# Optimization experiments

Hardware: AMD Instinct MI355X
Metric: run time of the kernel (lower is better)

The kernel has to match this reference:

```python
import jax, jax.numpy as jnp
import numpy as np
from jax import lax

H = 1028  # hidden_size


def _lstm_layer(x, w_ih, w_hh, b_ih, b_hh):
    # x: [B, T, in], w_ih: [4H, in], w_hh: [4H, H] (PyTorch gate order i,f,g,o)
    B, T, _ = x.shape
    h_dim = w_hh.shape[1]
    # Precompute input contribution for all timesteps (memory-bound GEMM)
    xg = jnp.einsum('bti,gi->btg', x, w_ih) + b_ih + b_hh  # [B, T, 4H]

    def step(carry, xt):
        h, c = carry
        g = xt + h @ w_hh.T  # [B, 4H]
        i, f, gg, o = jnp.split(g, 4, axis=-1)
        i = jax.nn.sigmoid(i)
        f = jax.nn.sigmoid(f)
        gg = jnp.tanh(gg)
        o = jax.nn.sigmoid(o)
        c = f * c + i * gg
        h = o * jnp.tanh(c)
        return (h, c), h

    h0 = jnp.zeros((B, h_dim), x.dtype)
    c0 = jnp.zeros((B, h_dim), x.dtype)
    _, hs = lax.scan(step, (h0, c0), jnp.swapaxes(xg, 0, 1))  # [T, B, H]
    return jnp.swapaxes(hs, 0, 1)  # [B, T, H]


def setup_inputs() -> dict:
    key = jax.random.key(0)
    ks = jax.random.split(key, 12)
    s = 1.0 / np.sqrt(H)  # torch LSTM/Linear init scale

    def u(k, shape):
        return jax.random.uniform(k, shape, jnp.float32, -s, s)

    x = jax.random.normal(ks[0], (1, 16384, 1), dtype=jnp.float32)
    return {
        'x': x,
        'w_ih0': u(ks[1], (4 * H, 1)),
        'w_hh0': u(ks[2], (4 * H, H)),
        'b_ih0': u(ks[3], (4 * H,)),
        'b_hh0': u(ks[4], (4 * H,)),
        'w_ih1': u(ks[5], (4 * H, H)),
        'w_hh1': u(ks[6], (4 * H, H)),
        'b_ih1': u(ks[7], (4 * H,)),
        'b_hh1': u(ks[8], (4 * H,)),
        'lin_w': u(ks[9], (1, H)),
        'lin_b': u(ks[10], (1,)),
    }


def reference(x, w_ih0, w_hh0, b_ih0, b_hh0, w_ih1, w_hh1, b_ih1, b_hh1, lin_w, lin_b):
    h1 = _lstm_layer(x, w_ih0, w_hh0, b_ih0, b_hh0)   # [B, T, H]
    h2 = _lstm_layer(h1, w_ih1, w_hh1, b_ih1, b_hh1)  # [B, T, H]
    return h2 @ lin_w.T + lin_b                        # [B, T, 1]
```

## Files before the change

kernel.cpp:

```cpp
#include <hip/hip_runtime.h>
#include <math.h>

#define HH    1028
#define TT    16384
#define UP    1056
#define HSU   1056
#define HS    1056
#define NWG0  66
#define NWG1  132
#define NWGT  (NWG0 + NWG1)
#define R0    1024
#define R0M   (R0 - 1)
#define R1M   15

typedef unsigned long long u64;

__device__ __forceinline__ u64 ld_u64(const u64* p) {
    return __hip_atomic_load(p, __ATOMIC_RELAXED, __HIP_MEMORY_SCOPE_AGENT);
}
__device__ __forceinline__ void st_u64(u64* p, u64 v) {
    __hip_atomic_store(p, v, __ATOMIC_RELAXED, __HIP_MEMORY_SCOPE_AGENT);
}
__device__ __forceinline__ unsigned ld_u32(const unsigned* p) {
    return __hip_atomic_load(p, __ATOMIC_RELAXED, __HIP_MEMORY_SCOPE_AGENT);
}
__device__ __forceinline__ void st_u32(unsigned* p, unsigned v) {
    __hip_atomic_store(p, v, __ATOMIC_RELAXED, __HIP_MEMORY_SCOPE_AGENT);
}
__device__ __forceinline__ float sigmf(float x) { return 1.0f / (1.0f + expf(-x)); }
__device__ __forceinline__ u64 pack(unsigned tag, float v) {
    return ((u64)tag << 32) | (u64)__float_as_uint(v);
}

__device__ __forceinline__ void stage132(const u64* __restrict__ src, float* __restrict__ lds,
                                         int base, int lane, unsigned want, long long& budget) {
    const int i0 = base + lane, i1 = base + 64 + lane, i2 = base + 128 + lane;
    bool d0 = false, d1 = false, d2 = (lane >= 4);
    for (;;) {
        if (!d0) { u64 v = ld_u64(src + i0);
                   if ((unsigned)(v >> 32) == want) { lds[i0] = __uint_as_float((unsigned)v); d0 = true; } }
        if (!d1) { u64 v = ld_u64(src + i1);
                   if ((unsigned)(v >> 32) == want) { lds[i1] = __uint_as_float((unsigned)v); d1 = true; } }
        if (!d2) { u64 v = ld_u64(src + i2);
                   if ((unsigned)(v >> 32) == want) { lds[i2] = __uint_as_float((unsigned)v); d2 = true; } }
        if (__all(d0 & d1 & d2)) break;
        if (--budget < 0) break;
        __builtin_amdgcn_s_sleep(1);
    }
}

__device__ __forceinline__ void stage264(const u64* __restrict__ src, float* __restrict__ lds,
                                         int base, int lane, unsigned want, long long& budget) {
    const int i0 = base + lane, i1 = i0 + 64, i2 = i0 + 128, i3 = i0 + 192, i4 = i0 + 256;
    bool d0 = false, d1 = false, d2 = false, d3 = false, d4 = (lane >= 8);
    for (;;) {
        if (!d0) { u64 v = ld_u64(src + i0);
                   if ((unsigned)(v >> 32) == want) { lds[i0] = __uint_as_float((unsigned)v); d0 = true; } }
        if (!d1) { u64 v = ld_u64(src + i1);
                   if ((unsigned)(v >> 32) == want) { lds[i1] = __uint_as_float((unsigned)v); d1 = true; } }
        if (!d2) { u64 v = ld_u64(src + i2);
                   if ((unsigned)(v >> 32) == want) { lds[i2] = __uint_as_float((unsigned)v); d2 = true; } }
        if (!d3) { u64 v = ld_u64(src + i3);
                   if ((unsigned)(v >> 32) == want) { lds[i3] = __uint_as_float((unsigned)v); d3 = true; } }
        if (!d4) { u64 v = ld_u64(src + i4);
                   if ((unsigned)(v >> 32) == want) { lds[i4] = __uint_as_float((unsigned)v); d4 = true; } }
        if (__all(d0 & d1 & d2 & d3 & d4)) break;
        if (--budget < 0) break;
        __builtin_amdgcn_s_sleep(1);
    }
}

__global__ __launch_bounds__(1024, 4) void wn_fused(
    const float* __restrict__ x,
    const float* __restrict__ w_ih0, const float* __restrict__ w_hh0,
    const float* __restrict__ b_ih0, const float* __restrict__ b_hh0,
    const float* __restrict__ w_ih1, const float* __restrict__ w_hh1,
    const float* __restrict__ b_ih1, const float* __restrict__ b_hh1,
    u64* __restrict__ ring0,
    u64* __restrict__ ring1,
    float* __restrict__ h2hist,
    unsigned* __restrict__ l1prog)
{
    __shared__ float smem[4 * UP + 128];
    const int tid  = threadIdx.x;
    const int lane = tid & 63;
    const int w    = tid >> 6;

    for (int i = tid; i < 4 * UP + 128; i += 1024) smem[i] = 0.0f;

    if (blockIdx.x < NWG0) {
        float* hbuf = smem;
        float* gbuf = smem + 2 * UP;
        const int wg   = blockIdx.x;
        const int row  = tid >> 4;
        const int k0   = tid & 15;
        const int gate = row >> 4;
        const int du   = row & 15;
        const int u    = wg * 16 + du;
        const bool real = (u < HH);
        const int wr   = gate * HH + (real ? u : 0);

        float wv[16][4], wt0 = 0.f, wt1 = 0.f;
#pragma unroll
        for (int m = 0; m < 16; ++m) {
            const int j = k0 * 4 + m * 64;
#pragma unroll
            for (int q = 0; q < 4; ++q)
                wv[m][q] = (real && j + q < HH) ? w_hh0[(size_t)wr * HH + j + q] : 0.0f;
        }
        {   const int j = 1024 + k0 * 2;
            wt0 = (real && j     < HH) ? w_hh0[(size_t)wr * HH + j]     : 0.0f;
            wt1 = (real && j + 1 < HH) ? w_hh0[(size_t)wr * HH + j + 1] : 0.0f; }
#pragma unroll
        for (int m = 0; m < 16; ++m)
#pragma unroll
            for (int q = 0; q < 4; ++q) asm volatile("" : "+v"(wv[m][q]));
        asm volatile("" : "+v"(wt0), "+v"(wt1));

        const float wx = real ? w_ih0[wr] : 0.0f;
        const float bs = real ? (b_ih0[wr] + b_hh0[wr]) : 0.0f;
        __syncthreads();

        long long budget = 20000000LL;
        float c_reg = 0.0f;
        for (int t = 0; t < TT; ++t) {
            if (t > 0) {
                if (w == 0) {
                    const float* gl = gbuf + ((t - 1) & 1) * 64;
                    if (lane < 16) {
                        const float gi = gl[lane], gf = gl[16 + lane];
                        const float gg = gl[32 + lane], go = gl[48 + lane];
                        const float iv = sigmf(gi), fv = sigmf(gf), gv = tanhf(gg), ov = sigmf(go);
                        c_reg = fv * c_reg + iv * gv;
                        float hv = ov * tanhf(c_reg);
                        if (wg * 16 + lane >= HH) hv = 0.0f;
                        st_u64(ring0 + (size_t)((t - 1) & R0M) * HSU + wg * 16 + lane,
                               pack((unsigned)t, hv));
                    }
                } else if (w >= 4 && w < 12) {
                    stage132(ring0 + (size_t)((t - 1) & R0M) * HSU, hbuf + (t & 1) * UP,
                             (w - 4) * 132, lane, (unsigned)t, budget);
                } else if (w == 1 && lane == 0 && (t & 255) == 0) {
                    for (;;) {
                        unsigned p = ld_u32(l1prog);
                        if ((int)t - (int)p < R0 - 256) break;
                        if (--budget < 0) break;
                        __builtin_amdgcn_s_sleep(32);
                    }
                }
            }
            __syncthreads();
            const float* hb = hbuf + (t & 1) * UP;
            float acc = 0.0f;
#pragma unroll
            for (int m = 0; m < 16; ++m) {
                const float4 hv = *(const float4*)&hb[k0 * 4 + m * 64];
                acc = fmaf(wv[m][0], hv.x, acc);
                acc = fmaf(wv[m][1], hv.y, acc);
                acc = fmaf(wv[m][2], hv.z, acc);
                acc = fmaf(wv[m][3], hv.w, acc);
            }
            {   const float2 hv = *(const float2*)&hb[1024 + k0 * 2];
                acc = fmaf(wt0, hv.x, acc);
                acc = fmaf(wt1, hv.y, acc); }
#pragma unroll
            for (int off = 1; off < 16; off <<= 1) acc += __shfl_xor(acc, off);
            if (k0 == 0) gbuf[(t & 1) * 64 + row] = acc + x[t] * wx + bs;
            __syncthreads();
        }
        if (w == 0 && lane < 16) {
            const float* gl = gbuf + ((TT - 1) & 1) * 64;
            const float gi = gl[lane], gf = gl[16 + lane];
            const float gg = gl[32 + lane], go = gl[48 + lane];
            const float iv = sigmf(gi), fv = sigmf(gf), gv = tanhf(gg), ov = sigmf(go);
            c_reg = fv * c_reg + iv * gv;
            float hv = ov * tanhf(c_reg);
            if (wg * 16 + lane >= HH) hv = 0.0f;
            st_u64(ring0 + (size_t)((TT - 1) & R0M) * HSU + wg * 16 + lane,
                   pack((unsigned)TT, hv));
        }
    } else {
        float* abuf = smem;
        float* bbuf = smem + 2 * UP;
        float* gbuf = smem + 4 * UP;
        const int wg   = blockIdx.x - NWG0;
        const int row  = tid >> 5;
        const int k0   = tid & 31;
        const int gate = row >> 3;
        const int du   = row & 7;
        const int u    = wg * 8 + du;
        const bool real = (u < HH);
        const int wr   = gate * HH + (real ? u : 0);

        float wiv[8][4], whv[8][4], wit = 0.f, wht = 0.f;
#pragma unroll
        for (int m = 0; m < 8; ++m) {
            const int j = k0 * 4 + m * 128;
#pragma unroll
            for (int q = 0; q < 4; ++q) {
                const bool inb = real && (j + q < HH);
                wiv[m][q] = inb ? w_ih1[(size_t)wr * HH + j + q] : 0.0f;
                whv[m][q] = inb ? w_hh1[(size_t)wr * HH + j + q] : 0.0f;
            }
        }
        {   const int j = 1024 + k0;
            wit = (real && j < HH) ? w_ih1[(size_t)wr * HH + j] : 0.0f;
            wht = (real && j < HH) ? w_hh1[(size_t)wr * HH + j] : 0.0f; }
#pragma unroll
        for (int m = 0; m < 8; ++m)
#pragma unroll
            for (int q = 0; q < 4; ++q) {
                asm volatile("" : "+v"(wiv[m][q]));
                asm volatile("" : "+v"(whv[m][q]));
            }
        asm volatile("" : "+v"(wit), "+v"(wht));
        const float bs = real ? (b_ih1[wr] + b_hh1[wr]) : 0.0f;
        __syncthreads();

        long long budget = 20000000LL;
        float c_reg = 0.0f;
        for (int t = 0; t < TT; ++t) {
            if (w == 0) {
                if (t > 0) {
                    const float* gl = gbuf + ((t - 1) & 1) * 32;
                    if (lane < 8) {
                        const float gi = gl[lane], gf = gl[8 + lane];
                        const float gg = gl[16 + lane], go = gl[24 + lane];
                        const float iv = sigmf(gi), fv = sigmf(gf), gv = tanhf(gg), ov = sigmf(go);
                        c_reg = fv * c_reg + iv * gv;
                        float hv = ov * tanhf(c_reg);
                        if (wg * 8 + lane >= HH) hv = 0.0f;
                        st_u64(ring1 + (size_t)((t - 1) & R1M) * HSU + wg * 8 + lane,
                               pack((unsigned)t, hv));
                        h2hist[(size_t)(t - 1) * HS + wg * 8 + lane] = hv;
                    }
                }
            } else if (w >= 4 && w < 12) {
                if (t > 0)
                    stage132(ring1 + (size_t)((t - 1) & R1M) * HSU, bbuf + (t & 1) * UP,
                             (w - 4) * 132, lane, (unsigned)t, budget);
            } else if (w >= 12) {
                stage264(ring0 + (size_t)(t & R0M) * HSU, abuf + (t & 1) * UP,
                         (w - 12) * 264, lane, (unsigned)(t + 1), budget);
            }
            __syncthreads();
            const float* ab = abuf + (t & 1) * UP;
            const float* bb = bbuf + (t & 1) * UP;
            float acc = 0.0f;
#pragma unroll
            for (int m = 0; m < 8; ++m) {
                const float4 ha = *(const float4*)&ab[k0 * 4 + m * 128];
                const float4 hb2 = *(const float4*)&bb[k0 * 4 + m * 128];
                acc = fmaf(wiv[m][0], ha.x, acc);
                acc = fmaf(wiv[m][1], ha.y, acc);
                acc = fmaf(wiv[m][2], ha.z, acc);
                acc = fmaf(wiv[m][3], ha.w, acc);
                acc = fmaf(whv[m][0], hb2.x, acc);
                acc = fmaf(whv[m][1], hb2.y, acc);
                acc = fmaf(whv[m][2], hb2.z, acc);
                acc = fmaf(whv[m][3], hb2.w, acc);
            }
            acc = fmaf(wit, ab[1024 + k0], acc);
            acc = fmaf(wht, bb[1024 + k0], acc);
#pragma unroll
            for (int off = 1; off < 32; off <<= 1) acc += __shfl_xor(acc, off);
            if (k0 == 0) gbuf[(t & 1) * 32 + row] = acc + bs;
            __syncthreads();
            if (w == 1 && lane == 0 && wg == 0 && (t & 255) == 255)
                st_u32(l1prog, (unsigned)(t + 1));
        }
        if (w == 0 && lane < 8) {
            const float* gl = gbuf + ((TT - 1) & 1) * 32;
            const float gi = gl[lane], gf = gl[8 + lane];
            const float gg = gl[16 + lane], go = gl[24 + lane];
            const float iv = sigmf(gi), fv = sigmf(gf), gv = tanhf(gg), ov = sigmf(go);
            c_reg = fv * c_reg + iv * gv;
            float hv = ov * tanhf(c_reg);
            if (wg * 8 + lane >= HH) hv = 0.0f;
            h2hist[(size_t)(TT - 1) * HS + wg * 8 + lane] = hv;
        }
    }
}

__global__ __launch_bounds__(256) void wn_proj(
    const float* __restrict__ h2,
    const float* __restrict__ lin_w,
    const float* __restrict__ lin_b,
    float* __restrict__ out)
{
    const int lane = threadIdx.x & 63;
    const int wv   = threadIdx.x >> 6;
    const int t    = blockIdx.x * 4 + wv;
    const float* hp = h2 + (size_t)t * HS;
    float acc = 0.0f;
#pragma unroll
    for (int m = 0; m < 4; ++m) {
        const int j = lane * 4 + m * 256;
        const float4 h4 = *(const float4*)(hp + j);
        const float4 w4 = *(const float4*)(lin_w + j);
        acc += h4.x * w4.x + h4.y * w4.y + h4.z * w4.z + h4.w * w4.w;
    }
    if (lane == 0) {
#pragma unroll
        for (int j = 1024; j < HH; ++j) acc += hp[j] * lin_w[j];
    }
#pragma unroll
    for (int off = 1; off < 64; off <<= 1) acc += __shfl_xor(acc, off);
    if (lane == 0) out[t] = acc + lin_b[0];
}

extern "C" void kernel_launch(void* const* d_in, const int* in_sizes, int n_in,
                              void* d_out, int out_size, void* d_ws, size_t ws_size,
                              hipStream_t stream) {
    const float* x     = (const float*)d_in[0];
    const float* w_ih0 = (const float*)d_in[1];
    const float* w_hh0 = (const float*)d_in[2];
    const float* b_ih0 = (const float*)d_in[3];
    const float* b_hh0 = (const float*)d_in[4];
    const float* w_ih1 = (const float*)d_in[5];
    const float* w_hh1 = (const float*)d_in[6];
    const float* b_ih1 = (const float*)d_in[7];
    const float* b_hh1 = (const float*)d_in[8];
    const float* lin_w = (const float*)d_in[9];
    const float* lin_b = (const float*)d_in[10];
    float* out = (float*)d_out;

    char* ws = (char*)d_ws;
    const size_t R0B = (size_t)R0 * HSU * 8;
    const size_t R1B = (size_t)16 * HSU * 8;
    const size_t H2B = (size_t)TT * HS * 4;
    u64* ring0 = (u64*)(ws);
    u64* ring1 = (u64*)(ws + R0B);
    float* h2hist = (float*)(ws + R0B + R1B);
    unsigned* l1prog = (unsigned*)(ws + R0B + R1B + H2B);

    wn_fused<<<NWGT, 1024, 0, stream>>>(x, w_ih0, w_hh0, b_ih0, b_hh0,
                                        w_ih1, w_hh1, b_ih1, b_hh1,
                                        ring0, ring1, h2hist, l1prog);
    wn_proj<<<TT / 4, 256, 0, stream>>>(h2hist, lin_w, lin_b, out);
}
```

Baseline: 43.45 ms.

## Halve workgroup size, compute LSTM cell per wave, publish h via LDS tag slots

Workgroups shrink from 1024 to 512 threads. Each wave now computes complete gate rows for its own hidden units (two units per wave in layer 0, one in layer 1) and evaluates the cell nonlinearity in-register with shuffles. This removes the gate buffer and the second __syncthreads per timestep, replacing it with tagged LDS slots that wave 0 polls before forwarding h to the global ring. All waves now share the staging of the ring into LDS. Each thread holds twice as many weight registers, and LDS spin-polling adds latency on the serial critical path.

After: 54.83 ms. +26.2%, slower.

```diff
diff --git a/kernel.cpp b/kernel.cpp
--- a/kernel.cpp
+++ b/kernel.cpp
@@ -26,6 +26,12 @@
 }
 __device__ __forceinline__ void st_u32(unsigned* p, unsigned v) {
     __hip_atomic_store(p, v, __ATOMIC_RELAXED, __HIP_MEMORY_SCOPE_AGENT);
+}
+__device__ __forceinline__ u64 lds_ld(const u64* p) {
+    return __hip_atomic_load(p, __ATOMIC_RELAXED, __HIP_MEMORY_SCOPE_WORKGROUP);
+}
+__device__ __forceinline__ void lds_st(u64* p, u64 v) {
+    __hip_atomic_store(p, v, __ATOMIC_RELAXED, __HIP_MEMORY_SCOPE_WORKGROUP);
 }
 __device__ __forceinline__ float sigmf(float x) { return 1.0f / (1.0f + expf(-x)); }
 __device__ __forceinline__ u64 pack(unsigned tag, float v) {
@@ -70,7 +76,20 @@
     }
 }
 
-__global__ __launch_bounds__(1024, 4) void wn_fused(
+__device__ __forceinline__ u64 gatherN(const u64* slots, int lane, int n, unsigned want,
+                                       long long& budget) {
+    u64 v = 0; bool done = (lane >= n);
+    for (;;) {
+        if (!done) { v = lds_ld(slots + lane);
+                     done = ((unsigned)(v >> 32) == want); }
+        if (__all(done)) break;
+        if (--budget < 0) break;
+        __builtin_amdgcn_s_sleep(1);
+    }
+    return v;
+}
+
+__global__ __launch_bounds__(512, 2) void wn_fused(
     const float* __restrict__ x,
     const float* __restrict__ w_ih0, const float* __restrict__ w_hh0,
     const float* __restrict__ b_ih0, const float* __restrict__ b_hh0,
@@ -81,66 +100,64 @@
     float* __restrict__ h2hist,
     unsigned* __restrict__ l1prog)
 {
-    __shared__ float smem[4 * UP + 128];
+    __shared__ float smem[4 * UP];
+    __shared__ u64 hslot[16];
     const int tid  = threadIdx.x;
     const int lane = tid & 63;
     const int w    = tid >> 6;
-
-    for (int i = tid; i < 4 * UP + 128; i += 1024) smem[i] = 0.0f;
+    const int gate = (lane >> 4) & 3;
+    const int k0   = lane & 15;
+
+    for (int i = tid; i < 4 * UP; i += 512) smem[i] = 0.0f;
+    if (tid < 16) hslot[tid] = 0;
 
     if (blockIdx.x < NWG0) {
         float* hbuf = smem;
-        float* gbuf = smem + 2 * UP;
-        const int wg   = blockIdx.x;
-        const int row  = tid >> 4;
-        const int k0   = tid & 15;
-        const int gate = row >> 4;
-        const int du   = row & 15;
-        const int u    = wg * 16 + du;
-        const bool real = (u < HH);
-        const int wr   = gate * HH + (real ? u : 0);
-
-        float wv[16][4], wt0 = 0.f, wt1 = 0.f;
+        const int wg = blockIdx.x;
+        const int u0 = wg * 16 + 2 * w;
+        const int u1 = u0 + 1;
+        const bool r0 = (u0 < HH), r1 = (u1 < HH);
+        const int wr0 = gate * HH + (r0 ? u0 : 0);
+        const int wr1 = gate * HH + (r1 ? u1 : 0);
+
+        float wa[16][4], wb[16][4], wta0 = 0.f, wta1 = 0.f, wtb0 = 0.f, wtb1 = 0.f;
 #pragma unroll
         for (int m = 0; m < 16; ++m) {
             const int j = k0 * 4 + m * 64;
 #pragma unroll
-            for (int q = 0; q < 4; ++q)
-                wv[m][q] = (real && j + q < HH) ? w_hh0[(size_t)wr * HH + j + q] : 0.0f;
+            for (int q = 0; q < 4; ++q) {
+                wa[m][q] = (r0 && j + q < HH) ? w_hh0[(size_t)wr0 * HH + j + q] : 0.0f;
+                wb[m][q] = (r1 && j + q < HH) ? w_hh0[(size_t)wr1 * HH + j + q] : 0.0f;
+            }
         }
         {   const int j = 1024 + k0 * 2;
-            wt0 = (real && j     < HH) ? w_hh0[(size_t)wr * HH + j]     : 0.0f;
-            wt1 = (real && j + 1 < HH) ? w_hh0[(size_t)wr * HH + j + 1] : 0.0f; }
+            wta0 = (r0 && j     < HH) ? w_hh0[(size_t)wr0 * HH + j]     : 0.0f;
+            wta1 = (r0 && j + 1 < HH) ? w_hh0[(size_t)wr0 * HH + j + 1] : 0.0f;
+            wtb0 = (r1 && j     < HH) ? w_hh0[(size_t)wr1 * HH + j]     : 0.0f;
+            wtb1 = (r1 && j + 1 < HH) ? w_hh0[(size_t)wr1 * HH + j + 1] : 0.0f; }
 #pragma unroll
         for (int m = 0; m < 16; ++m)
 #pragma unroll
-            for (int q = 0; q < 4; ++q) asm volatile("" : "+v"(wv[m][q]));
-        asm volatile("" : "+v"(wt0), "+v"(wt1));
-
-        const float wx = real ? w_ih0[wr] : 0.0f;
-        const float bs = real ? (b_ih0[wr] + b_hh0[wr]) : 0.0f;
+            for (int q = 0; q < 4; ++q) {
+                asm volatile("" : "+v"(wa[m][q]));
+                asm volatile("" : "+v"(wb[m][q]));
+            }
+        asm volatile("" : "+v"(wta0), "+v"(wta1), "+v"(wtb0), "+v"(wtb1));
+
+        const float wx0 = r0 ? w_ih0[wr0] : 0.0f;
+        const float bs0 = r0 ? (b_ih0[wr0] + b_hh0[wr0]) : 0.0f;
+        const float wx1 = r1 ? w_ih0[wr1] : 0.0f;
+        const float bs1 = r1 ? (b_ih0[wr1] + b_hh0[wr1]) : 0.0f;
         __syncthreads();
 
         long long budget = 20000000LL;
-        float c_reg = 0.0f;
+        float c0 = 0.0f, c1 = 0.0f;
         for (int t = 0; t < TT; ++t) {
             if (t > 0) {
                 if (w == 0) {
-                    const float* gl = gbuf + ((t - 1) & 1) * 64;
-                    if (lane < 16) {
-                        const float gi = gl[lane], gf = gl[16 + lane];
-                        const float gg = gl[32 + lane], go = gl[48 + lane];
-                        const float iv = sigmf(gi), fv = sigmf(gf), gv = tanhf(gg), ov = sigmf(go);
-                        c_reg = fv * c_reg + iv * gv;
-                        float hv = ov * tanhf(c_reg);
-                        if (wg * 16 + lane >= HH) hv = 0.0f;
-                        st_u64(ring0 + (size_t)((t - 1) & R0M) * HSU + wg * 16 + lane,
-                               pack((unsigned)t, hv));
-                    }
-                } else if (w >= 4 && w < 12) {
-                    stage132(ring0 + (size_t)((t - 1) & R0M) * HSU, hbuf + (t & 1) * UP,
-                             (w - 4) * 132, lane, (unsigned)t, budget);
-                } else if (w == 1 && lane == 0 && (t & 255) == 0) {
+                    u64 v = gatherN(hslot, lane, 16, (unsigned)t, budget);
+                    if (lane < 16) st_u64(ring0 + (size_t)((t - 1) & R0M) * HSU + wg * 16 + lane, v);
+                } else if (w == 1 && lane == 63 && (t & 255) == 0) {
                     for (;;) {
                         unsigned p = ld_u32(l1prog);
                         if ((int)t - (int)p < R0 - 256) break;
@@ -148,54 +165,72 @@
                         __builtin_amdgcn_s_sleep(32);
                     }
                 }
+                stage132(ring0 + (size_t)((t - 1) & R0M) * HSU, hbuf + (t & 1) * UP,
+                         w * 132, lane, (unsigned)t, budget);
             }
             __syncthreads();
             const float* hb = hbuf + (t & 1) * UP;
-            float acc = 0.0f;
+            float a0 = 0.0f, a1 = 0.0f;
 #pragma unroll
             for (int m = 0; m < 16; ++m) {
                 const float4 hv = *(const float4*)&hb[k0 * 4 + m * 64];
-                acc = fmaf(wv[m][0], hv.x, acc);
-                acc = fmaf(wv[m][1], hv.y, acc);
-                acc = fmaf(wv[m][2], hv.z, acc);
-                acc = fmaf(wv[m][3], hv.w, acc);
+                a0 = fmaf(wa[m][0], hv.x, a0);
+                a0 = fmaf(wa[m][1], hv.y, a0);
+                a0 = fmaf(wa[m][2], hv.z, a0);
+                a0 = fmaf(wa[m][3], hv.w, a0);
+                a1 = fmaf(wb[m][0], hv.x, a1);
+                a1 = fmaf(wb[m][1], hv.y, a1);
+                a1 = fmaf(wb[m][2], hv.z, a1);
+                a1 = fmaf(wb[m][3], hv.w, a1);
             }
             {   const float2 hv = *(const float2*)&hb[1024 + k0 * 2];
-                acc = fmaf(wt0, hv.x, acc);
-                acc = fmaf(wt1, hv.y, acc); }
-#pragma unroll
-            for (int off = 1; off < 16; off <<= 1) acc += __shfl_xor(acc, off);
-            if (k0 == 0) gbuf[(t & 1) * 64 + row] = acc + x[t] * wx + bs;
-            __syncthreads();
-        }
-        if (w == 0 && lane < 16) {
-            const float* gl = gbuf + ((TT - 1) & 1) * 64;
-            const float gi = gl[lane], gf = gl[16 + lane];
-            const float gg = gl[32 + lane], go = gl[48 + lane];
-            const float iv = sigmf(gi), fv = sigmf(gf), gv = tanhf(gg), ov = sigmf(go);
-            c_reg = fv * c_reg + iv * gv;
-            float hv = ov * tanhf(c_reg);
-            if (wg * 16 + lane >= HH) hv = 0.0f;
-            st_u64(ring0 + (size_t)((TT - 1) & R0M) * HSU + wg * 16 + lane,
-                   pack((unsigned)TT, hv));
+                a0 = fmaf(wta0, hv.x, a0);
+                a0 = fmaf(wta1, hv.y, a0);
+                a1 = fmaf(wtb0, hv.x, a1);
+                a1 = fmaf(wtb1, hv.y, a1); }
+#pragma unroll
+            for (int off = 1; off < 16; off <<= 1) {
+                a0 += __shfl_xor(a0, off);
+                a1 += __shfl_xor(a1, off);
+            }
+            const float xt = x[t];
+            if (k0 == 0) {
+                a0 += xt * wx0 + bs0;
+                a1 += xt * wx1 + bs1;
+            }
+            {   const float gi = __shfl(a0, 0),  gf = __shfl(a0, 16);
+                const float gg = __shfl(a0, 32), go = __shfl(a0, 48);
+                const float iv = sigmf(gi), fv = sigmf(gf), gv = tanhf(gg), ov = sigmf(go);
+                c0 = fv * c0 + iv * gv;
+                float hv0 = ov * tanhf(c0);
+                if (!r0) hv0 = 0.0f;
+                if (lane == 0) lds_st(&hslot[2 * w], pack((unsigned)(t + 1), hv0));
+            }
+            {   const float gi = __shfl(a1, 0),  gf = __shfl(a1, 16);
+                const float gg = __shfl(a1, 32), go = __shfl(a1, 48);
+                const float iv = sigmf(gi), fv = sigmf(gf), gv = tanhf(gg), ov = sigmf(go);
+                c1 = fv * c1 + iv * gv;
+                float hv1 = ov * tanhf(c1);
+                if (!r1) hv1 = 0.0f;
+                if (lane == 0) lds_st(&hslot[2 * w + 1], pack((unsigned)(t + 1), hv1));
+            }
+        }
+        if (w == 0) {
+            u64 v = gatherN(hslot, lane, 16, (unsigned)TT, budget);
+            if (lane < 16) st_u64(ring0 + (size_t)((TT - 1) & R0M) * HSU + wg * 16 + lane, v);
         }
     } else {
         float* abuf = smem;
         float* bbuf = smem + 2 * UP;
-        float* gbuf = smem + 4 * UP;
-        const int wg   = blockIdx.x - NWG0;
-        const int row  = tid >> 5;
-        const int k0   = tid & 31;
-        const int gate = row >> 3;
-        const int du   = row & 7;
-        const int u    = wg * 8 + du;
+        const int wg = blockIdx.x - NWG0;
+        const int u  = wg * 8 + w;
         const bool real = (u < HH);
-        const int wr   = gate * HH + (real ? u : 0);
-
-        float wiv[8][4], whv[8][4], wit = 0.f, wht = 0.f;
-#pragma unroll
-        for (int m = 0; m < 8; ++m) {
-            const int j = k0 * 4 + m * 128;
+        const int wr = gate * HH + (real ? u : 0);
+
+        float wiv[16][4], whv[16][4], wi0 = 0.f, wi1 = 0.f, wh0 = 0.f, wh1 = 0.f;
+#pragma unroll
+        for (int m = 0; m < 16; ++m) {
+            const int j = k0 * 4 + m * 64;
 #pragma unroll
             for (int q = 0; q < 4; ++q) {
                 const bool inb = real && (j + q < HH);
@@ -203,81 +238,82 @@
                 whv[m][q] = inb ? w_hh1[(size_t)wr * HH + j + q] : 0.0f;
             }
         }
-        {   const int j = 1024 + k0;
-            wit = (real && j < HH) ? w_ih1[(size_t)wr * HH + j] : 0.0f;
-            wht = (real && j < HH) ? w_hh1[(size_t)wr * HH + j] : 0.0f; }
-#pragma unroll
-        for (int m = 0; m < 8; ++m)
+        {   const int j = 1024 + k0 * 2;
+            wi0 = (real && j     < HH) ? w_ih1[(size_t)wr * HH + j]     : 0.0f;
+            wi1 = (real && j + 1 < HH) ? w_ih1[(size_t)wr * HH + j + 1] : 0.0f;
+            wh0 = (real && j     < HH) ? w_hh1[(size_t)wr * HH + j]     : 0.0f;
+            wh1 = (real && j + 1 < HH) ? w_hh1[(size_t)wr * HH + j + 1] : 0.0f; }
+#pragma unroll
+        for (int m = 0; m < 16; ++m)
 #pragma unroll
             for (int q = 0; q < 4; ++q) {
                 asm volatile("" : "+v"(wiv[m][q]));
                 asm volatile("" : "+v"(whv[m][q]));
             }
-        asm volatile("" : "+v"(wit), "+v"(wht));
+        asm volatile("" : "+v"(wi0), "+v"(wi1), "+v"(wh0), "+v"(wh1));
         const float bs = real ? (b_ih1[wr] + b_hh1[wr]) : 0.0f;
         __syncthreads();
 
         long long budget = 20000000LL;
         float c_reg = 0.0f;
         for (int t = 0; t < TT; ++t) {
-            if (w == 0) {
-                if (t > 0) {
-                    const float* gl = gbuf + ((t - 1) & 1) * 32;
-                    if (lane < 8) {
-                        const float gi = gl[lane], gf = gl[8 + lane];
-                        const float gg = gl[16 + lane], go = gl[24 + lane];
-                        const float iv = sigmf(gi), fv = sigmf(gf), gv = tanhf(gg), ov = sigmf(go);
-                        c_reg = fv * c_reg + iv * gv;
-                        float hv = ov * tanhf(c_reg);
-                        if (wg * 8 + lane >= HH) hv = 0.0f;
-                        st_u64(ring1 + (size_t)((t - 1) & R1M) * HSU + wg * 8 + lane,
-                               pack((unsigned)t, hv));
-                        h2hist[(size_t)(t - 1) * HS + wg * 8 + lane] = hv;
-                    }
+            if (w == 0 && t > 0) {
+                u64 v = gatherN(hslot, lane, 8, (unsigned)t, budget);
+                if (lane < 8) {
+                    st_u64(ring1 + (size_t)((t - 1) & R1M) * HSU + wg * 8 + lane, v);
+                    h2hist[(size_t)(t - 1) * HS + wg * 8 + lane] = __uint_as_float((unsigned)v);
                 }
-            } else if (w >= 4 && w < 12) {
+            }
+            if (w < 4) {
                 if (t > 0)
-                    stage132(ring1 + (size_t)((t - 1) & R1M) * HSU, bbuf + (t & 1) * UP,
-                             (w - 4) * 132, lane, (unsigned)t, budget);
-            } else if (w >= 12) {
+                    stage264(ring1 + (size_t)((t - 1) & R1M) * HSU, bbuf + (t & 1) * UP,
+                             w * 264, lane, (unsigned)t, budget);
+            } else {
                 stage264(ring0 + (size_t)(t & R0M) * HSU, abuf + (t & 1) * UP,
-                         (w - 12) * 264, lane, (unsigned)(t + 1), budget);
+                         (w - 4) * 264, lane, (unsigned)(t + 1), budget);
             }
             __syncthreads();
             const float* ab = abuf + (t & 1) * UP;
             const float* bb = bbuf + (t & 1) * UP;
             float acc = 0.0f;
 #pragma unroll
-            for (int m = 0; m < 8; ++m) {
-                const float4 ha = *(const float4*)&ab[k0 * 4 + m * 128];
-                const float4 hb2 = *(const float4*)&bb[k0 * 4 + m * 128];
+            for (int m = 0; m < 16; ++m) {
+                const float4 ha = *(const float4*)&ab[k0 * 4 + m * 64];
+                const float4 hb = *(const float4*)&bb[k0 * 4 + m * 64];
                 acc = fmaf(wiv[m][0], ha.x, acc);
                 acc = fmaf(wiv[m][1], ha.y, acc);
                 acc = fmaf(wiv[m][2], ha.z, acc);
                 acc = fmaf(wiv[m][3], ha.w, acc);
-                acc = fmaf(whv[m][0], hb2.x, acc);
-                acc = fmaf(whv[m][1], hb2.y, acc);
-                acc = fmaf(whv[m][2], hb2.z, acc);
-                acc = fmaf(whv[m][3], hb2.w, acc);
-            }
-            acc = fmaf(wit, ab[1024 + k0], acc);
-            acc = fmaf(wht, bb[1024 + k0], acc);
-#pragma unroll
-            for (int off = 1; off < 32; off <<= 1) acc += __shfl_xor(acc, off);
-            if (k0 == 0) gbuf[(t & 1) * 32 + row] = acc + bs;
-            __syncthreads();
-            if (w == 1 && lane == 0 && wg == 0 && (t & 255) == 255)
-                st_u32(l1prog, (unsigned)(t + 1));
-        }
-        if (w == 0 && lane < 8) {
-            const float* gl = gbuf + ((TT - 1) & 1) * 32;
-            const float gi = gl[lane], gf = gl[8 + lane];
-            const float gg = gl[16 + lane], go = gl[24 + lane];
+                acc = fmaf(whv[m][0], hb.x, acc);
+                acc = fmaf(whv[m][1], hb.y, acc);
+                acc = fmaf(whv[m][2], hb.z, acc);
+                acc = fmaf(whv[m][3], hb.w, acc);
+            }
+            {   const float2 ha = *(const float2*)&ab[1024 + k0 * 2];
+                const float2 hb = *(const float2*)&bb[1024 + k0 * 2];
+                acc = fmaf(wi0, ha.x, acc);
+                acc = fmaf(wi1, ha.y, acc);
+                acc = fmaf(wh0, hb.x, acc);
+                acc = fmaf(wh1, hb.y, acc); }
+#pragma unroll
+            for (int off = 1; off < 16; off <<= 1) acc += __shfl_xor(acc, off);
+            if (k0 == 0) acc += bs;
+            const float gi = __shfl(acc, 0);
+            const float gf = __shfl(acc, 16);
+            const float gg = __shfl(acc, 32);
+            const float go = __shfl(acc, 48);
             const float iv = sigmf(gi), fv = sigmf(gf), gv = tanhf(gg), ov = sigmf(go);
             c_reg = fv * c_reg + iv * gv;
             float hv = ov * tanhf(c_reg);
-            if (wg * 8 + lane >= HH) hv = 0.0f;
-            h2hist[(size_t)(TT - 1) * HS + wg * 8 + lane] = hv;
+            if (!real) hv = 0.0f;
+            if (lane == 0) lds_st(&hslot[w], pack((unsigned)(t + 1), hv));
+            if (w == 7 && lane == 63 && wg == 0 && (t & 255) == 255)
+                st_u32(l1prog, (unsigned)(t + 1));
+        }
+        if (w == 0) {
+            u64 v = gatherN(hslot, lane, 8, (unsigned)TT, budget);
+            if (lane < 8)
+                h2hist[(size_t)(TT - 1) * HS + wg * 8 + lane] = __uint_as_float((unsigned)v);
         }
     }
 }
@@ -334,8 +370,8 @@
     float* h2hist = (float*)(ws + R0B + R1B);
     unsigned* l1prog = (unsigned*)(ws + R0B + R1B + H2B);
 
-    wn_fused<<<NWGT, 1024, 0, stream>>>(x, w_ih0, w_hh0, b_ih0, b_hh0,
-                                        w_ih1, w_hh1, b_ih1, b_hh1,
-                                        ring0, ring1, h2hist, l1prog);
+    wn_fused<<<NWGT, 512, 0, stream>>>(x, w_ih0, w_hh0, b_ih0, b_hh0,
+                                       w_ih1, w_hh1, b_ih1, b_hh1,
+                                       ring0, ring1, h2hist, l1prog);
     wn_proj<<<TT / 4, 256, 0, stream>>>(h2hist, lin_w, lin_b, out);
 }
```

## Replace second per-step barrier with tagged LDS gate slots and widen staging

Applied to the files above, without the earlier changes.

Drops the second __syncthreads per timestep in both LSTM layers. Gate sums are now written as tag+value 64-bit words into LDS slots, and wave 0 spin-polls those slots and gathers the gates with shuffles. Staging of the global h ring is spread over 11 waves with 96 elements each instead of 8 waves with 132, and the l1prog progress store moves to a staging wave. The aim is to cut the barrier latency on the serial recurrence critical path. The cost is LDS polling and a greater reliance on relaxed workgroup-scope ordering to stay correct.

Result: no change. 43.66 ms (+0.5%).

```diff
diff --git a/kernel.cpp b/kernel.cpp
--- a/kernel.cpp
+++ b/kernel.cpp
@@ -27,23 +27,27 @@
 __device__ __forceinline__ void st_u32(unsigned* p, unsigned v) {
     __hip_atomic_store(p, v, __ATOMIC_RELAXED, __HIP_MEMORY_SCOPE_AGENT);
 }
+__device__ __forceinline__ u64 lds_ld(const u64* p) {
+    return __hip_atomic_load(p, __ATOMIC_RELAXED, __HIP_MEMORY_SCOPE_WORKGROUP);
+}
+__device__ __forceinline__ void lds_st(u64* p, u64 v) {
+    __hip_atomic_store(p, v, __ATOMIC_RELAXED, __HIP_MEMORY_SCOPE_WORKGROUP);
+}
 __device__ __forceinline__ float sigmf(float x) { return 1.0f / (1.0f + expf(-x)); }
 __device__ __forceinline__ u64 pack(unsigned tag, float v) {
     return ((u64)tag << 32) | (u64)__float_as_uint(v);
 }
 
-__device__ __forceinline__ void stage132(const u64* __restrict__ src, float* __restrict__ lds,
-                                         int base, int lane, unsigned want, long long& budget) {
-    const int i0 = base + lane, i1 = base + 64 + lane, i2 = base + 128 + lane;
-    bool d0 = false, d1 = false, d2 = (lane >= 4);
+__device__ __forceinline__ void stage96(const u64* __restrict__ src, float* __restrict__ lds,
+                                        int base, int lane, unsigned want, long long& budget) {
+    const int i0 = base + lane, i1 = base + 64 + lane;
+    bool d0 = false, d1 = (lane >= 32);
     for (;;) {
         if (!d0) { u64 v = ld_u64(src + i0);
                    if ((unsigned)(v >> 32) == want) { lds[i0] = __uint_as_float((unsigned)v); d0 = true; } }
         if (!d1) { u64 v = ld_u64(src + i1);
                    if ((unsigned)(v >> 32) == want) { lds[i1] = __uint_as_float((unsigned)v); d1 = true; } }
-        if (!d2) { u64 v = ld_u64(src + i2);
-                   if ((unsigned)(v >> 32) == want) { lds[i2] = __uint_as_float((unsigned)v); d2 = true; } }
-        if (__all(d0 & d1 & d2)) break;
+        if (__all(d0 & d1)) break;
         if (--budget < 0) break;
         __builtin_amdgcn_s_sleep(1);
     }
@@ -70,6 +74,19 @@
     }
 }
 
+__device__ __forceinline__ float pollslots(const u64* slots, int lane, int n, unsigned want,
+                                           long long& budget) {
+    u64 v = 0; bool done = (lane >= n);
+    for (;;) {
+        if (!done) { v = lds_ld(slots + lane);
+                     done = ((unsigned)(v >> 32) == want); }
+        if (__all(done)) break;
+        if (--budget < 0) break;
+        __builtin_amdgcn_s_sleep(1);
+    }
+    return __uint_as_float((unsigned)v);
+}
+
 __global__ __launch_bounds__(1024, 4) void wn_fused(
     const float* __restrict__ x,
     const float* __restrict__ w_ih0, const float* __restrict__ w_hh0,
@@ -81,16 +98,17 @@
     float* __restrict__ h2hist,
     unsigned* __restrict__ l1prog)
 {
-    __shared__ float smem[4 * UP + 128];
+    __shared__ float smem[4 * UP];
+    __shared__ u64 gslot[2 * 64];
     const int tid  = threadIdx.x;
     const int lane = tid & 63;
     const int w    = tid >> 6;
 
-    for (int i = tid; i < 4 * UP + 128; i += 1024) smem[i] = 0.0f;
+    for (int i = tid; i < 4 * UP; i += 1024) smem[i] = 0.0f;
+    if (tid < 128) gslot[tid] = 0;
 
     if (blockIdx.x < NWG0) {
         float* hbuf = smem;
-        float* gbuf = smem + 2 * UP;
         const int wg   = blockIdx.x;
         const int row  = tid >> 4;
         const int k0   = tid & 15;
@@ -126,10 +144,12 @@
         for (int t = 0; t < TT; ++t) {
             if (t > 0) {
                 if (w == 0) {
-                    const float* gl = gbuf + ((t - 1) & 1) * 64;
+                    float gsum = pollslots(gslot + ((t - 1) & 1) * 64, lane, 64, (unsigned)t, budget);
+                    const float gi = __shfl(gsum, lane & 15);
+                    const float gf = __shfl(gsum, 16 + (lane & 15));
+                    const float gg = __shfl(gsum, 32 + (lane & 15));
+                    const float go = __shfl(gsum, 48 + (lane & 15));
                     if (lane < 16) {
-                        const float gi = gl[lane], gf = gl[16 + lane];
-                        const float gg = gl[32 + lane], go = gl[48 + lane];
                         const float iv = sigmf(gi), fv = sigmf(gf), gv = tanhf(gg), ov = sigmf(go);
                         c_reg = fv * c_reg + iv * gv;
                         float hv = ov * tanhf(c_reg);
@@ -137,10 +157,10 @@
                         st_u64(ring0 + (size_t)((t - 1) & R0M) * HSU + wg * 16 + lane,
                                pack((unsigned)t, hv));
                     }
-                } else if (w >= 4 && w < 12) {
-                    stage132(ring0 + (size_t)((t - 1) & R0M) * HSU, hbuf + (t & 1) * UP,
-                             (w - 4) * 132, lane, (unsigned)t, budget);
-                } else if (w == 1 && lane == 0 && (t & 255) == 0) {
+                } else if (w >= 1 && w < 12) {
+                    stage96(ring0 + (size_t)((t - 1) & R0M) * HSU, hbuf + (t & 1) * UP,
+                            (w - 1) * 96, lane, (unsigned)t, budget);
+                } else if (w == 12 && lane == 0 && (t & 255) == 0) {
                     for (;;) {
                         unsigned p = ld_u32(l1prog);
                         if ((int)t - (int)p < R0 - 256) break;
@@ -165,24 +185,28 @@
                 acc = fmaf(wt1, hv.y, acc); }
 #pragma unroll
             for (int off = 1; off < 16; off <<= 1) acc += __shfl_xor(acc, off);
-            if (k0 == 0) gbuf[(t & 1) * 64 + row] = acc + x[t] * wx + bs;
-            __syncthreads();
-        }
-        if (w == 0 && lane < 16) {
-            const float* gl = gbuf + ((TT - 1) & 1) * 64;
-            const float gi = gl[lane], gf = gl[16 + lane];
-            const float gg = gl[32 + lane], go = gl[48 + lane];
-            const float iv = sigmf(gi), fv = sigmf(gf), gv = tanhf(gg), ov = sigmf(go);
-            c_reg = fv * c_reg + iv * gv;
-            float hv = ov * tanhf(c_reg);
-            if (wg * 16 + lane >= HH) hv = 0.0f;
-            st_u64(ring0 + (size_t)((TT - 1) & R0M) * HSU + wg * 16 + lane,
-                   pack((unsigned)TT, hv));
+            if (k0 == 0)
+                lds_st(&gslot[(t & 1) * 64 + row],
+                       pack((unsigned)(t + 1), acc + x[t] * wx + bs));
+        }
+        if (w == 0) {
+            float gsum = pollslots(gslot + ((TT - 1) & 1) * 64, lane, 64, (unsigned)TT, budget);
+            const float gi = __shfl(gsum, lane & 15);
+            const float gf = __shfl(gsum, 16 + (lane & 15));
+            const float gg = __shfl(gsum, 32 + (lane & 15));
+            const float go = __shfl(gsum, 48 + (lane & 15));
+            if (lane < 16) {
+                const float iv = sigmf(gi), fv = sigmf(gf), gv = tanhf(gg), ov = sigmf(go);
+                c_reg = fv * c_reg + iv * gv;
+                float hv = ov * tanhf(c_reg);
+                if (wg * 16 + lane >= HH) hv = 0.0f;
+                st_u64(ring0 + (size_t)((TT - 1) & R0M) * HSU + wg * 16 + lane,
+                       pack((unsigned)TT, hv));
+            }
         }
     } else {
         float* abuf = smem;
         float* bbuf = smem + 2 * UP;
-        float* gbuf = smem + 4 * UP;
         const int wg   = blockIdx.x - NWG0;
         const int row  = tid >> 5;
         const int k0   = tid & 31;
@@ -222,10 +246,12 @@
         for (int t = 0; t < TT; ++t) {
             if (w == 0) {
                 if (t > 0) {
-                    const float* gl = gbuf + ((t - 1) & 1) * 32;
+                    float gsum = pollslots(gslot + ((t - 1) & 1) * 32, lane, 32, (unsigned)t, budget);
+                    const float gi = __shfl(gsum, lane & 7);
+                    const float gf = __shfl(gsum, 8 + (lane & 7));
+                    const float gg = __shfl(gsum, 16 + (lane & 7));
+                    const float go = __shfl(gsum, 24 + (lane & 7));
                     if (lane < 8) {
-                        const float gi = gl[lane], gf = gl[8 + lane];
-                        const float gg = gl[16 + lane], go = gl[24 + lane];
                         const float iv = sigmf(gi), fv = sigmf(gf), gv = tanhf(gg), ov = sigmf(go);
                         c_reg = fv * c_reg + iv * gv;
                         float hv = ov * tanhf(c_reg);
@@ -235,13 +261,15 @@
                         h2hist[(size_t)(t - 1) * HS + wg * 8 + lane] = hv;
                     }
                 }
-            } else if (w >= 4 && w < 12) {
+            } else if (w < 12) {
                 if (t > 0)
-                    stage132(ring1 + (size_t)((t - 1) & R1M) * HSU, bbuf + (t & 1) * UP,
-                             (w - 4) * 132, lane, (unsigned)t, budget);
-            } else if (w >= 12) {
+                    stage96(ring1 + (size_t)((t - 1) & R1M) * HSU, bbuf + (t & 1) * UP,
+                            (w - 1) * 96, lane, (unsigned)t, budget);
+            } else {
                 stage264(ring0 + (size_t)(t & R0M) * HSU, abuf + (t & 1) * UP,
                          (w - 12) * 264, lane, (unsigned)(t + 1), budget);
+                if (w == 15 && lane == 63 && wg == 0 && (t & 255) == 255)
+                    st_u32(l1prog, (unsigned)(t + 1));
             }
             __syncthreads();
             const float* ab = abuf + (t & 1) * UP;
@@ -264,20 +292,22 @@
             acc = fmaf(wht, bb[1024 + k0], acc);
 #pragma unroll
             for (int off = 1; off < 32; off <<= 1) acc += __shfl_xor(acc, off);
-            if (k0 == 0) gbuf[(t & 1) * 32 + row] = acc + bs;
-            __syncthreads();
-            if (w == 1 && lane == 0 && wg == 0 && (t & 255) == 255)
-                st_u32(l1prog, (unsigned)(t + 1));
-        }
-        if (w == 0 && lane < 8) {
-            const float* gl = gbuf + ((TT - 1) & 1) * 32;
-            const float gi = gl[lane], gf = gl[8 + lane];
-            const float gg = gl[16 + lane], go = gl[24 + lane];
-            const float iv = sigmf(gi), fv = sigmf(gf), gv = tanhf(gg), ov = sigmf(go);
-            c_reg = fv * c_reg + iv * gv;
-            float hv = ov * tanhf(c_reg);
-            if (wg * 8 + lane >= HH) hv = 0.0f;
-            h2hist[(size_t)(TT - 1) * HS + wg * 8 + lane] = hv;
+            if (k0 == 0)
+                lds_st(&gslot[(t & 1) * 32 + row], pack((unsigned)(t + 1), acc + bs));
+        }
+        if (w == 0) {
+            float gsum = pollslots(gslot + ((TT - 1) & 1) * 32, lane, 32, (unsigned)TT, budget);
+            const float gi = __shfl(gsum, lane & 7);
+            const float gf = __shfl(gsum, 8 + (lane & 7));
+            const float gg = __shfl(gsum, 16 + (lane & 7));
+            const float go = __shfl(gsum, 24 + (lane & 7));
+            if (lane < 8) {
+                const float iv = sigmf(gi), fv = sigmf(gf), gv = tanhf(gg), ov = sigmf(go);
+                c_reg = fv * c_reg + iv * gv;
+                float hv = ov * tanhf(c_reg);
+                if (wg * 8 + lane >= HH) hv = 0.0f;
+                h2hist[(size_t)(TT - 1) * HS + wg * 8 + lane] = hv;
+            }
         }
     }
 }
```
